# Optimization experiments

Hardware: AMD Instinct MI355X
Metric: run time of the kernel (lower is better)

## Reference

```python
import jax, jax.numpy as jnp
import numpy as np

PAD = 3            # ConstantPad1d padding
PAD_VAL = -1.0     # ConstantPad1d value
STRIDE = 1
POOL = 2           # pool_size == pool_stride == 2
BN_EPS = 1e-5


def setup_inputs() -> dict:
    key = jax.random.key(0)
    k1, k2 = jax.random.split(key)
    x = jax.random.normal(k1, (256, 64, 4096), dtype=jnp.float32)
    W = jax.random.normal(k2, (128, 64, 7), dtype=jnp.float32)
    alpha = jnp.ones((1,), dtype=jnp.float32) * 0.25   # nn.PReLU default init
    gamma = jnp.ones((128,), dtype=jnp.float32)
    beta = jnp.zeros((128,), dtype=jnp.float32)
    return {"x": x, "W": W, "alpha": alpha, "gamma": gamma, "beta": beta}


def reference(x, W, alpha, gamma, beta):
    # 1) constant pad with value PAD_VAL along length
    xp = jnp.pad(x, ((0, 0), (0, 0), (PAD, PAD)), constant_values=PAD_VAL)
    # 2) binarize activations and weights (sign; sign(0)=0 as in torch)
    ba = jnp.sign(xp)
    bw = jnp.sign(W)
    # 3) float conv1d on +/-1 values, no bias  -> [B, Cout, L]
    y = jax.lax.conv_general_dilated(
        ba, bw, window_strides=(STRIDE,), padding='VALID',
        dimension_numbers=('NCW', 'OIW', 'NCW'))
    # 4) max pool k=2, s=2 (non-overlapping -> reshape trick)
    B, C, L = y.shape
    y = y[:, :, : (L // POOL) * POOL].reshape(B, C, L // POOL, POOL).max(axis=-1)
    # 5) PReLU with single shared alpha
    y = jnp.where(y > 0, y, alpha[0] * y)
    # 6) BatchNorm1d in training mode: batch stats over (B, L), biased variance
    mean = jnp.mean(y, axis=(0, 2), keepdims=True)
    var = jnp.mean((y - mean) ** 2, axis=(0, 2), keepdims=True)
    y = (y - mean) * jax.lax.rsqrt(var + BN_EPS)
    y = y * gamma[None, :, None] + beta[None, :, None]
    return y
```

## Files before the change

### kernel.cpp

```cpp
#include <hip/hip_runtime.h>
#include <stdint.h>

#define BATCH 256
#define CIN   64
#define LIN   4096
#define PADN  3
#define LPAD  4102
#define COUT  128
#define KW    7
#define LPOOL 2048
#define NBUCKET 64
#define NPERCH (256LL * 2048LL)

typedef unsigned long long u64;
typedef __attribute__((ext_vector_type(4)))  int i32x4;
typedef __attribute__((ext_vector_type(16))) int i32x16;

#define ACC_ZERO {0,0,0,0,0,0,0,0,0,0,0,0,0,0,0,0}

__global__ __launch_bounds__(256) void pack_x_kernel(const float* __restrict__ x,
                                                     char* __restrict__ sx,
                                                     int b_base)
{
    const int t  = threadIdx.x;
    const int lt = blockIdx.x;
    const int bl = blockIdx.y;
    const int b  = b_base + bl;
    const int l  = lt * 256 + t;
    const float* xb = x + (size_t)b * CIN * LIN + l;

    int o[16];
    #pragma unroll
    for (int cw = 0; cw < 16; ++cw) {
        unsigned wv = 0;
        #pragma unroll
        for (int j = 0; j < 4; ++j) {
            float v = xb[(size_t)(cw * 4 + j) * LIN];
            unsigned s = (v > 0.0f) ? 1u : ((v < 0.0f) ? 0xFFu : 0u);
            wv |= s << (8 * j);
        }
        o[cw] = (int)wv;
    }
    i32x4* dst = (i32x4*)(sx + ((size_t)bl * LPAD + (l + PADN)) * 64);
    dst[0] = (i32x4){o[0],  o[1],  o[2],  o[3]};
    dst[1] = (i32x4){o[4],  o[5],  o[6],  o[7]};
    dst[2] = (i32x4){o[8],  o[9],  o[10], o[11]};
    dst[3] = (i32x4){o[12], o[13], o[14], o[15]};

    const i32x4 ff = (i32x4){-1, -1, -1, -1};
    if (lt == 0 && t < PADN) {
        i32x4* pd = (i32x4*)(sx + ((size_t)bl * LPAD + t) * 64);
        pd[0] = ff; pd[1] = ff; pd[2] = ff; pd[3] = ff;
    }
    if (lt == 15 && t < PADN) {
        i32x4* pd = (i32x4*)(sx + ((size_t)bl * LPAD + (LIN + PADN) + t) * 64);
        pd[0] = ff; pd[1] = ff; pd[2] = ff; pd[3] = ff;
    }
}

__global__ __launch_bounds__(256) void pack_w_kernel(const float* __restrict__ w,
                                                     char* __restrict__ pwb)
{
    int idx = blockIdx.x * 256 + threadIdx.x;
    if (idx >= KW * COUT * CIN) return;
    int kk = idx >> 13;
    int co = (idx >> 6) & 127;
    int c  = idx & 63;
    float v = w[((size_t)co * CIN + c) * KW + kk];
    pwb[idx] = (char)((v > 0.0f) ? 1 : ((v < 0.0f) ? -1 : 0));
}


__global__ __launch_bounds__(256, 2) void conv_stats_kernel(
    const char* __restrict__ sx, const char* __restrict__ pwb,
    u64* __restrict__ stats, int b_base)
{
    const int tid  = threadIdx.x;
    const int lane = tid & 63;
    const int w    = tid >> 6;
    const int ngrp = w & 1;
    const int mgrp = w >> 1;
    const int col  = lane & 31;
    const int hi   = lane >> 5;
    const int bl   = blockIdx.y;
    const int mchunk = blockIdx.x;

    const char* sxb = sx + (size_t)bl * LPAD * 64;
    const char* wb0 = pwb + (size_t)((ngrp * 64 + col) * 64) + hi * 16;

    int sp0=0, sn0=0, qp0=0, qn0=0, sp1=0, sn1=0, qp1=0, qn1=0;

    for (int mt = 0; mt < 4; ++mt) {
        const int q0 = mchunk * 256 + mgrp * 128 + mt * 32;
        i32x16 a00 = ACC_ZERO, a01 = ACC_ZERO, a10 = ACC_ZERO, a11 = ACC_ZERO;
        #pragma unroll
        for (int kk = 0; kk < KW; ++kk) {
            const char* ar = sxb + (size_t)(q0 + col + kk) * 64;
            i32x4 x0 = *(const i32x4*)(ar + hi * 16);
            i32x4 x1 = *(const i32x4*)(ar + 32 + hi * 16);
            const char* wk = wb0 + (size_t)kk * (COUT * 64);
            i32x4 w00 = *(const i32x4*)(wk);
            i32x4 w01 = *(const i32x4*)(wk + 32);
            i32x4 w10 = *(const i32x4*)(wk + 2048);
            i32x4 w11 = *(const i32x4*)(wk + 2048 + 32);
            a00 = __builtin_amdgcn_mfma_i32_32x32x32_i8(x0, w00, a00, 0, 0, 0);
            a01 = __builtin_amdgcn_mfma_i32_32x32x32_i8(x1, w01, a01, 0, 0, 0);
            a10 = __builtin_amdgcn_mfma_i32_32x32x32_i8(x0, w10, a10, 0, 0, 0);
            a11 = __builtin_amdgcn_mfma_i32_32x32x32_i8(x1, w11, a11, 0, 0, 0);
        }
        i32x16 acc0 = a00 + a01;
        i32x16 acc1 = a10 + a11;
        #pragma unroll
        for (int r = 0; r < 8; ++r) {
            int p = acc0[2*r] > acc0[2*r+1] ? acc0[2*r] : acc0[2*r+1];
            int q = p * p;
            bool pos = p > 0;
            sp0 += pos ? p : 0;  sn0 += pos ? 0 : p;
            qp0 += pos ? q : 0;  qn0 += pos ? 0 : q;
            p = acc1[2*r] > acc1[2*r+1] ? acc1[2*r] : acc1[2*r+1];
            q = p * p;
            pos = p > 0;
            sp1 += pos ? p : 0;  sn1 += pos ? 0 : p;
            qp1 += pos ? q : 0;  qn1 += pos ? 0 : q;
        }
    }

    sp0 += __shfl_xor(sp0, 32);  sn0 += __shfl_xor(sn0, 32);
    qp0 += __shfl_xor(qp0, 32);  qn0 += __shfl_xor(qn0, 32);
    sp1 += __shfl_xor(sp1, 32);  sn1 += __shfl_xor(sn1, 32);
    qp1 += __shfl_xor(qp1, 32);  qn1 += __shfl_xor(qn1, 32);

    if (hi == 0) {
        const int bkt = (b_base + bl) & (NBUCKET - 1);
        u64* s0 = stats + (size_t)(bkt * COUT + ngrp * 64 + col) * 4;
        atomicAdd(&s0[0], (u64)(long long)sp0);
        atomicAdd(&s0[1], (u64)(long long)sn0);
        atomicAdd(&s0[2], (u64)(long long)qp0);
        atomicAdd(&s0[3], (u64)(long long)qn0);
        u64* s1 = stats + (size_t)(bkt * COUT + ngrp * 64 + 32 + col) * 4;
        atomicAdd(&s1[0], (u64)(long long)sp1);
        atomicAdd(&s1[1], (u64)(long long)sn1);
        atomicAdd(&s1[2], (u64)(long long)qp1);
        atomicAdd(&s1[3], (u64)(long long)qn1);
    }
}

__global__ void finalize_kernel(const u64* __restrict__ stats,
                                const float* __restrict__ alpha,
                                const float* __restrict__ gamma,
                                const float* __restrict__ beta,
                                float2* __restrict__ scsh)
{
    int c = threadIdx.x;
    if (c >= COUT) return;
    long long s[4] = {0, 0, 0, 0};
    for (int bk = 0; bk < NBUCKET; ++bk)
        #pragma unroll
        for (int i = 0; i < 4; ++i)
            s[i] += (long long)stats[(size_t)(bk * COUT + c) * 4 + i];
    double a    = (double)alpha[0];
    double N    = (double)NPERCH;
    double sum  = (double)s[0] + a * (double)s[1];
    double ssq  = (double)s[2] + a * a * (double)s[3];
    double mean = sum / N;
    double var  = ssq / N - mean * mean;
    double inv  = 1.0 / sqrt(var + 1e-5);
    double g    = (double)gamma[c];
    scsh[c] = make_float2((float)(g * inv),
                          (float)((double)beta[c] - mean * g * inv));
}

__global__ __launch_bounds__(256, 2) void conv_write_kernel(
    const char* __restrict__ sx, const char* __restrict__ pwb,
    const float2* __restrict__ scsh, const float* __restrict__ alpha,
    float* __restrict__ out, int b_base)
{
    const int tid  = threadIdx.x;
    const int lane = tid & 63;
    const int w    = tid >> 6;
    const int ngrp = w & 1;
    const int mgrp = w >> 1;
    const int col  = lane & 31;
    const int hi   = lane >> 5;
    const int bl   = blockIdx.y;
    const int mchunk = blockIdx.x;

    const char* sxb = sx + (size_t)bl * LPAD * 64;
    const char* wb0 = pwb + (size_t)((ngrp * 64 + col) * 64) + hi * 16;

    const float a = alpha[0];
    const float2 ss0 = scsh[ngrp * 64 + col];
    const float2 ss1 = scsh[ngrp * 64 + 32 + col];
    const int gb = b_base + bl;
    float* orow0 = out + ((size_t)gb * COUT + ngrp * 64 + col) * LPOOL;
    float* orow1 = orow0 + (size_t)32 * LPOOL;

    for (int mt = 0; mt < 4; ++mt) {
        const int q0 = mchunk * 256 + mgrp * 128 + mt * 32;
        i32x16 a00 = ACC_ZERO, a01 = ACC_ZERO, a10 = ACC_ZERO, a11 = ACC_ZERO;
        #pragma unroll
        for (int kk = 0; kk < KW; ++kk) {
            const char* ar = sxb + (size_t)(q0 + col + kk) * 64;
            i32x4 x0 = *(const i32x4*)(ar + hi * 16);
            i32x4 x1 = *(const i32x4*)(ar + 32 + hi * 16);
            const char* wk = wb0 + (size_t)kk * (COUT * 64);
            i32x4 w00 = *(const i32x4*)(wk);
            i32x4 w01 = *(const i32x4*)(wk + 32);
            i32x4 w10 = *(const i32x4*)(wk + 2048);
            i32x4 w11 = *(const i32x4*)(wk + 2048 + 32);
            a00 = __builtin_amdgcn_mfma_i32_32x32x32_i8(x0, w00, a00, 0, 0, 0);
            a01 = __builtin_amdgcn_mfma_i32_32x32x32_i8(x1, w01, a01, 0, 0, 0);
            a10 = __builtin_amdgcn_mfma_i32_32x32x32_i8(x0, w10, a10, 0, 0, 0);
            a11 = __builtin_amdgcn_mfma_i32_32x32x32_i8(x1, w11, a11, 0, 0, 0);
        }
        i32x16 acc0 = a00 + a01;
        i32x16 acc1 = a10 + a11;
        const int lp0 = q0 >> 1;
        #pragma unroll
        for (int r = 0; r < 8; ++r) {
            const int prow = (r & 1) + 4 * (r >> 1) + 2 * hi;
            int p = acc0[2*r] > acc0[2*r+1] ? acc0[2*r] : acc0[2*r+1];
            float y = (p > 0) ? (float)p : a * (float)p;
            orow0[lp0 + prow] = fmaf(y, ss0.x, ss0.y);
            p = acc1[2*r] > acc1[2*r+1] ? acc1[2*r] : acc1[2*r+1];
            y = (p > 0) ? (float)p : a * (float)p;
            orow1[lp0 + prow] = fmaf(y, ss1.x, ss1.y);
        }
    }
}

extern "C" void kernel_launch(void* const* d_in, const int* in_sizes, int n_in,
                              void* d_out, int out_size, void* d_ws, size_t ws_size,
                              hipStream_t stream)
{
    const float* x     = (const float*)d_in[0];
    const float* W     = (const float*)d_in[1];
    const float* alpha = (const float*)d_in[2];
    const float* gamma = (const float*)d_in[3];
    const float* beta  = (const float*)d_in[4];
    float* out = (float*)d_out;

    const size_t PER_B    = (size_t)LPAD * 64;
    const size_t pwb_sz   = (size_t)KW * COUT * CIN;
    const size_t stats_sz = (size_t)NBUCKET * COUT * 4 * 8;
    const size_t scsh_sz  = (size_t)COUT * 8;
    const size_t fixed    = pwb_sz + stats_sz + scsh_sz + 1024;

    int nb = BATCH;
    if (ws_size < PER_B * BATCH + fixed) {
        size_t avail = (ws_size > fixed) ? (ws_size - fixed) : PER_B;
        nb = (int)(avail / PER_B);
        if (nb < 1) nb = 1;
        if (nb > BATCH) nb = BATCH;
    }

    char* ws = (char*)d_ws;
    char* sx = ws;
    size_t off = ((PER_B * (size_t)nb) + 255) & ~(size_t)255;
    char* pwb = ws + off;               off = (off + pwb_sz + 255) & ~(size_t)255;
    u64* stats = (u64*)(ws + off);      off = (off + stats_sz + 255) & ~(size_t)255;
    float2* scsh = (float2*)(ws + off);

    hipMemsetAsync(stats, 0, stats_sz, stream);
    pack_w_kernel<<<dim3(224), 256, 0, stream>>>(W, pwb);

    for (int b0 = 0; b0 < BATCH; b0 += nb) {
        int n = (BATCH - b0 < nb) ? (BATCH - b0) : nb;
        pack_x_kernel<<<dim3(16, n), 256, 0, stream>>>(x, sx, b0);
        conv_stats_kernel<<<dim3(16, n), 256, 0, stream>>>(sx, pwb, stats, b0);
    }
    finalize_kernel<<<dim3(1), 128, 0, stream>>>(stats, alpha, gamma, beta, scsh);

    if (nb == BATCH) {
        conv_write_kernel<<<dim3(16, BATCH), 256, 0, stream>>>(sx, pwb, scsh, alpha, out, 0);
    } else {
        for (int b0 = 0; b0 < BATCH; b0 += nb) {
            int n = (BATCH - b0 < nb) ? (BATCH - b0) : nb;
            pack_x_kernel<<<dim3(16, n), 256, 0, stream>>>(x, sx, b0);
            conv_write_kernel<<<dim3(16, n), 256, 0, stream>>>(sx, pwb, scsh, alpha, out, b0);
        }
    }
}
```

Measured before the change: 396.3 us.

## Store pooled int16 conv results to skip second convolution pass

When the workspace is large enough, the stats pass now also writes the max-pooled integer conv results as int16 into a buffer. A separate elementwise kernel then applies PReLU and the BatchNorm scale and shift, so the whole binary convolution is no longer recomputed just to write the output. It also merges the split accumulators into one chain per output tile and raises the occupancy hint to three blocks. The cost is about 134MB of extra int16 writes and reads plus scattered 2-byte stores from the MFMA layout, and it needs a larger workspace.

```diff
diff --git a/kernel.cpp b/kernel.cpp
--- a/kernel.cpp
+++ b/kernel.cpp
@@ -15,6 +15,7 @@
 typedef unsigned long long u64;
 typedef __attribute__((ext_vector_type(4)))  int i32x4;
 typedef __attribute__((ext_vector_type(16))) int i32x16;
+typedef __attribute__((ext_vector_type(8)))  short s16x8;
 
 #define ACC_ZERO {0,0,0,0,0,0,0,0,0,0,0,0,0,0,0,0}
 
@@ -70,10 +71,10 @@
     pwb[idx] = (char)((v > 0.0f) ? 1 : ((v < 0.0f) ? -1 : 0));
 }
 
-
-__global__ __launch_bounds__(256, 2) void conv_stats_kernel(
+template<int STOREP>
+__global__ __launch_bounds__(256, 3) void conv_stats_kernel(
     const char* __restrict__ sx, const char* __restrict__ pwb,
-    u64* __restrict__ stats, int b_base)
+    u64* __restrict__ stats, short* __restrict__ pstore, int b_base)
 {
     const int tid  = threadIdx.x;
     const int lane = tid & 63;
@@ -88,7 +89,147 @@
     const char* sxb = sx + (size_t)bl * LPAD * 64;
     const char* wb0 = pwb + (size_t)((ngrp * 64 + col) * 64) + hi * 16;
 
+    const int gb = b_base + bl;
+    short* prow0 = STOREP ? (pstore + ((size_t)gb * COUT + ngrp * 64 + col) * LPOOL)
+                          : (short*)nullptr;
+    short* prow1 = STOREP ? (prow0 + (size_t)32 * LPOOL) : (short*)nullptr;
+
     int sp0=0, sn0=0, qp0=0, qn0=0, sp1=0, sn1=0, qp1=0, qn1=0;
+
+    for (int mt = 0; mt < 4; ++mt) {
+        const int q0 = mchunk * 256 + mgrp * 128 + mt * 32;
+        i32x16 acc0 = ACC_ZERO, acc1 = ACC_ZERO;
+        #pragma unroll
+        for (int kk = 0; kk < KW; ++kk) {
+            const char* ar = sxb + (size_t)(q0 + col + kk) * 64;
+            i32x4 x0 = *(const i32x4*)(ar + hi * 16);
+            i32x4 x1 = *(const i32x4*)(ar + 32 + hi * 16);
+            const char* wk = wb0 + (size_t)kk * (COUT * 64);
+            i32x4 w00 = *(const i32x4*)(wk);
+            i32x4 w01 = *(const i32x4*)(wk + 32);
+            i32x4 w10 = *(const i32x4*)(wk + 2048);
+            i32x4 w11 = *(const i32x4*)(wk + 2048 + 32);
+            acc0 = __builtin_amdgcn_mfma_i32_32x32x32_i8(x0, w00, acc0, 0, 0, 0);
+            acc0 = __builtin_amdgcn_mfma_i32_32x32x32_i8(x1, w01, acc0, 0, 0, 0);
+            acc1 = __builtin_amdgcn_mfma_i32_32x32x32_i8(x0, w10, acc1, 0, 0, 0);
+            acc1 = __builtin_amdgcn_mfma_i32_32x32x32_i8(x1, w11, acc1, 0, 0, 0);
+        }
+        const int lp0 = q0 >> 1;
+        #pragma unroll
+        for (int r = 0; r < 8; ++r) {
+            int p = acc0[2*r] > acc0[2*r+1] ? acc0[2*r] : acc0[2*r+1];
+            int q = p * p;
+            bool pos = p > 0;
+            sp0 += pos ? p : 0;  sn0 += pos ? 0 : p;
+            qp0 += pos ? q : 0;  qn0 += pos ? 0 : q;
+            int p1 = acc1[2*r] > acc1[2*r+1] ? acc1[2*r] : acc1[2*r+1];
+            int q1 = p1 * p1;
+            bool pos1 = p1 > 0;
+            sp1 += pos1 ? p1 : 0;  sn1 += pos1 ? 0 : p1;
+            qp1 += pos1 ? q1 : 0;  qn1 += pos1 ? 0 : q1;
+            if (STOREP) {
+                const int prow = (r & 1) + 4 * (r >> 1) + 2 * hi;
+                prow0[lp0 + prow] = (short)p;
+                prow1[lp0 + prow] = (short)p1;
+            }
+        }
+    }
+
+    sp0 += __shfl_xor(sp0, 32);  sn0 += __shfl_xor(sn0, 32);
+    qp0 += __shfl_xor(qp0, 32);  qn0 += __shfl_xor(qn0, 32);
+    sp1 += __shfl_xor(sp1, 32);  sn1 += __shfl_xor(sn1, 32);
+    qp1 += __shfl_xor(qp1, 32);  qn1 += __shfl_xor(qn1, 32);
+
+    if (hi == 0) {
+        const int bkt = gb & (NBUCKET - 1);
+        u64* s0 = stats + (size_t)(bkt * COUT + ngrp * 64 + col) * 4;
+        atomicAdd(&s0[0], (u64)(long long)sp0);
+        atomicAdd(&s0[1], (u64)(long long)sn0);
+        atomicAdd(&s0[2], (u64)(long long)qp0);
+        atomicAdd(&s0[3], (u64)(long long)qn0);
+        u64* s1 = stats + (size_t)(bkt * COUT + ngrp * 64 + 32 + col) * 4;
+        atomicAdd(&s1[0], (u64)(long long)sp1);
+        atomicAdd(&s1[1], (u64)(long long)sn1);
+        atomicAdd(&s1[2], (u64)(long long)qp1);
+        atomicAdd(&s1[3], (u64)(long long)qn1);
+    }
+}
+
+__global__ void finalize_kernel(const u64* __restrict__ stats,
+                                const float* __restrict__ alpha,
+                                const float* __restrict__ gamma,
+                                const float* __restrict__ beta,
+                                float2* __restrict__ scsh)
+{
+    int c = threadIdx.x;
+    if (c >= COUT) return;
+    long long s[4] = {0, 0, 0, 0};
+    for (int bk = 0; bk < NBUCKET; ++bk)
+        #pragma unroll
+        for (int i = 0; i < 4; ++i)
+            s[i] += (long long)stats[(size_t)(bk * COUT + c) * 4 + i];
+    double a    = (double)alpha[0];
+    double N    = (double)NPERCH;
+    double sum  = (double)s[0] + a * (double)s[1];
+    double ssq  = (double)s[2] + a * a * (double)s[3];
+    double mean = sum / N;
+    double var  = ssq / N - mean * mean;
+    double inv  = 1.0 / sqrt(var + 1e-5);
+    double g    = (double)gamma[c];
+    scsh[c] = make_float2((float)(g * inv),
+                          (float)((double)beta[c] - mean * g * inv));
+}
+
+__global__ __launch_bounds__(256) void bn_write_kernel(
+    const short* __restrict__ p, const float2* __restrict__ scsh,
+    const float* __restrict__ alpha, float* __restrict__ out)
+{
+    const float a = alpha[0];
+    const size_t i = ((size_t)blockIdx.x * 256 + threadIdx.x) * 8;
+    const int co = (int)((i >> 11) & (COUT - 1));
+    const float2 ss = scsh[co];
+    const s16x8 v = *(const s16x8*)(p + i);
+    float4 o0, o1;
+    #pragma unroll
+    for (int j = 0; j < 4; ++j) {
+        float pv = (float)v[j];
+        float y = (pv > 0.0f) ? pv : a * pv;
+        ((float*)&o0)[j] = fmaf(y, ss.x, ss.y);
+    }
+    #pragma unroll
+    for (int j = 0; j < 4; ++j) {
+        float pv = (float)v[4 + j];
+        float y = (pv > 0.0f) ? pv : a * pv;
+        ((float*)&o1)[j] = fmaf(y, ss.x, ss.y);
+    }
+    *(float4*)(out + i)     = o0;
+    *(float4*)(out + i + 4) = o1;
+}
+
+__global__ __launch_bounds__(256, 2) void conv_write_kernel(
+    const char* __restrict__ sx, const char* __restrict__ pwb,
+    const float2* __restrict__ scsh, const float* __restrict__ alpha,
+    float* __restrict__ out, int b_base)
+{
+    const int tid  = threadIdx.x;
+    const int lane = tid & 63;
+    const int w    = tid >> 6;
+    const int ngrp = w & 1;
+    const int mgrp = w >> 1;
+    const int col  = lane & 31;
+    const int hi   = lane >> 5;
+    const int bl   = blockIdx.y;
+    const int mchunk = blockIdx.x;
+
+    const char* sxb = sx + (size_t)bl * LPAD * 64;
+    const char* wb0 = pwb + (size_t)((ngrp * 64 + col) * 64) + hi * 16;
+
+    const float a = alpha[0];
+    const float2 ss0 = scsh[ngrp * 64 + col];
+    const float2 ss1 = scsh[ngrp * 64 + 32 + col];
+    const int gb = b_base + bl;
+    float* orow0 = out + ((size_t)gb * COUT + ngrp * 64 + col) * LPOOL;
+    float* orow1 = orow0 + (size_t)32 * LPOOL;
 
     for (int mt = 0; mt < 4; ++mt) {
         const int q0 = mchunk * 256 + mgrp * 128 + mt * 32;
@@ -110,111 +251,6 @@
         }
         i32x16 acc0 = a00 + a01;
         i32x16 acc1 = a10 + a11;
-        #pragma unroll
-        for (int r = 0; r < 8; ++r) {
-            int p = acc0[2*r] > acc0[2*r+1] ? acc0[2*r] : acc0[2*r+1];
-            int q = p * p;
-            bool pos = p > 0;
-            sp0 += pos ? p : 0;  sn0 += pos ? 0 : p;
-            qp0 += pos ? q : 0;  qn0 += pos ? 0 : q;
-            p = acc1[2*r] > acc1[2*r+1] ? acc1[2*r] : acc1[2*r+1];
-            q = p * p;
-            pos = p > 0;
-            sp1 += pos ? p : 0;  sn1 += pos ? 0 : p;
-            qp1 += pos ? q : 0;  qn1 += pos ? 0 : q;
-        }
-    }
-
-    sp0 += __shfl_xor(sp0, 32);  sn0 += __shfl_xor(sn0, 32);
-    qp0 += __shfl_xor(qp0, 32);  qn0 += __shfl_xor(qn0, 32);
-    sp1 += __shfl_xor(sp1, 32);  sn1 += __shfl_xor(sn1, 32);
-    qp1 += __shfl_xor(qp1, 32);  qn1 += __shfl_xor(qn1, 32);
-
-    if (hi == 0) {
-        const int bkt = (b_base + bl) & (NBUCKET - 1);
-        u64* s0 = stats + (size_t)(bkt * COUT + ngrp * 64 + col) * 4;
-        atomicAdd(&s0[0], (u64)(long long)sp0);
-        atomicAdd(&s0[1], (u64)(long long)sn0);
-        atomicAdd(&s0[2], (u64)(long long)qp0);
-        atomicAdd(&s0[3], (u64)(long long)qn0);
-        u64* s1 = stats + (size_t)(bkt * COUT + ngrp * 64 + 32 + col) * 4;
-        atomicAdd(&s1[0], (u64)(long long)sp1);
-        atomicAdd(&s1[1], (u64)(long long)sn1);
-        atomicAdd(&s1[2], (u64)(long long)qp1);
-        atomicAdd(&s1[3], (u64)(long long)qn1);
-    }
-}
-
-__global__ void finalize_kernel(const u64* __restrict__ stats,
-                                const float* __restrict__ alpha,
-                                const float* __restrict__ gamma,
-                                const float* __restrict__ beta,
-                                float2* __restrict__ scsh)
-{
-    int c = threadIdx.x;
-    if (c >= COUT) return;
-    long long s[4] = {0, 0, 0, 0};
-    for (int bk = 0; bk < NBUCKET; ++bk)
-        #pragma unroll
-        for (int i = 0; i < 4; ++i)
-            s[i] += (long long)stats[(size_t)(bk * COUT + c) * 4 + i];
-    double a    = (double)alpha[0];
-    double N    = (double)NPERCH;
-    double sum  = (double)s[0] + a * (double)s[1];
-    double ssq  = (double)s[2] + a * a * (double)s[3];
-    double mean = sum / N;
-    double var  = ssq / N - mean * mean;
-    double inv  = 1.0 / sqrt(var + 1e-5);
-    double g    = (double)gamma[c];
-    scsh[c] = make_float2((float)(g * inv),
-                          (float)((double)beta[c] - mean * g * inv));
-}
-
-__global__ __launch_bounds__(256, 2) void conv_write_kernel(
-    const char* __restrict__ sx, const char* __restrict__ pwb,
-    const float2* __restrict__ scsh, const float* __restrict__ alpha,
-    float* __restrict__ out, int b_base)
-{
-    const int tid  = threadIdx.x;
-    const int lane = tid & 63;
-    const int w    = tid >> 6;
-    const int ngrp = w & 1;
-    const int mgrp = w >> 1;
-    const int col  = lane & 31;
-    const int hi   = lane >> 5;
-    const int bl   = blockIdx.y;
-    const int mchunk = blockIdx.x;
-
-    const char* sxb = sx + (size_t)bl * LPAD * 64;
-    const char* wb0 = pwb + (size_t)((ngrp * 64 + col) * 64) + hi * 16;
-
-    const float a = alpha[0];
-    const float2 ss0 = scsh[ngrp * 64 + col];
-    const float2 ss1 = scsh[ngrp * 64 + 32 + col];
-    const int gb = b_base + bl;
-    float* orow0 = out + ((size_t)gb * COUT + ngrp * 64 + col) * LPOOL;
-    float* orow1 = orow0 + (size_t)32 * LPOOL;
-
-    for (int mt = 0; mt < 4; ++mt) {
-        const int q0 = mchunk * 256 + mgrp * 128 + mt * 32;
-        i32x16 a00 = ACC_ZERO, a01 = ACC_ZERO, a10 = ACC_ZERO, a11 = ACC_ZERO;
-        #pragma unroll
-        for (int kk = 0; kk < KW; ++kk) {
-            const char* ar = sxb + (size_t)(q0 + col + kk) * 64;
-            i32x4 x0 = *(const i32x4*)(ar + hi * 16);
-            i32x4 x1 = *(const i32x4*)(ar + 32 + hi * 16);
-            const char* wk = wb0 + (size_t)kk * (COUT * 64);
-            i32x4 w00 = *(const i32x4*)(wk);
-            i32x4 w01 = *(const i32x4*)(wk + 32);
-            i32x4 w10 = *(const i32x4*)(wk + 2048);
-            i32x4 w11 = *(const i32x4*)(wk + 2048 + 32);
-            a00 = __builtin_amdgcn_mfma_i32_32x32x32_i8(x0, w00, a00, 0, 0, 0);
-            a01 = __builtin_amdgcn_mfma_i32_32x32x32_i8(x1, w01, a01, 0, 0, 0);
-            a10 = __builtin_amdgcn_mfma_i32_32x32x32_i8(x0, w10, a10, 0, 0, 0);
-            a11 = __builtin_amdgcn_mfma_i32_32x32x32_i8(x1, w11, a11, 0, 0, 0);
-        }
-        i32x16 acc0 = a00 + a01;
-        i32x16 acc1 = a10 + a11;
         const int lp0 = q0 >> 1;
         #pragma unroll
         for (int r = 0; r < 8; ++r) {
@@ -240,12 +276,33 @@
     const float* beta  = (const float*)d_in[4];
     float* out = (float*)d_out;
 
-    const size_t PER_B    = (size_t)LPAD * 64;
+    const size_t sx_sz    = (size_t)BATCH * LPAD * 64;
+    const size_t p_sz     = (size_t)BATCH * COUT * LPOOL * 2;
     const size_t pwb_sz   = (size_t)KW * COUT * CIN;
     const size_t stats_sz = (size_t)NBUCKET * COUT * 4 * 8;
     const size_t scsh_sz  = (size_t)COUT * 8;
-    const size_t fixed    = pwb_sz + stats_sz + scsh_sz + 1024;
-
+    const size_t fixed    = pwb_sz + stats_sz + scsh_sz + 4096;
+
+    char* ws = (char*)d_ws;
+
+    if (ws_size >= sx_sz + p_sz + fixed) {
+        char* sx = ws;
+        size_t off = (sx_sz + 255) & ~(size_t)255;
+        short* p = (short*)(ws + off);       off = (off + p_sz + 255) & ~(size_t)255;
+        char* pwb = ws + off;                off = (off + pwb_sz + 255) & ~(size_t)255;
+        u64* stats = (u64*)(ws + off);       off = (off + stats_sz + 255) & ~(size_t)255;
+        float2* scsh = (float2*)(ws + off);
+
+        hipMemsetAsync(stats, 0, stats_sz, stream);
+        pack_w_kernel<<<dim3(224), 256, 0, stream>>>(W, pwb);
+        pack_x_kernel<<<dim3(16, BATCH), 256, 0, stream>>>(x, sx, 0);
+        conv_stats_kernel<1><<<dim3(16, BATCH), 256, 0, stream>>>(sx, pwb, stats, p, 0);
+        finalize_kernel<<<dim3(1), 128, 0, stream>>>(stats, alpha, gamma, beta, scsh);
+        bn_write_kernel<<<dim3(32768), 256, 0, stream>>>(p, scsh, alpha, out);
+        return;
+    }
+
+    const size_t PER_B = (size_t)LPAD * 64;
     int nb = BATCH;
     if (ws_size < PER_B * BATCH + fixed) {
         size_t avail = (ws_size > fixed) ? (ws_size - fixed) : PER_B;
@@ -254,7 +311,6 @@
         if (nb > BATCH) nb = BATCH;
     }
 
-    char* ws = (char*)d_ws;
     char* sx = ws;
     size_t off = ((PER_B * (size_t)nb) + 255) & ~(size_t)255;
     char* pwb = ws + off;               off = (off + pwb_sz + 255) & ~(size_t)255;
@@ -267,7 +323,7 @@
     for (int b0 = 0; b0 < BATCH; b0 += nb) {
         int n = (BATCH - b0 < nb) ? (BATCH - b0) : nb;
         pack_x_kernel<<<dim3(16, n), 256, 0, stream>>>(x, sx, b0);
-        conv_stats_kernel<<<dim3(16, n), 256, 0, stream>>>(sx, pwb, stats, b0);
+        conv_stats_kernel<0><<<dim3(16, n), 256, 0, stream>>>(sx, pwb, stats, nullptr, b0);
     }
     finalize_kernel<<<dim3(1), 128, 0, stream>>>(stats, alpha, gamma, beta, scsh);
 
```

After: 388.4 us. 2.0% less time.
